# Optimization experiments

Hardware: AMD Instinct MI355X
Metric: run time of the kernel (lower is better)

Reference implementation:

```python
import jax, jax.numpy as jnp
import numpy as np

B, J, O = 32, 20, 20
D, H, F, L = 256, 8, 1024, 6
S = J * O
DH = D // H
NL = L + 1  # 6 encoder blocks + final block stacked together


def setup_inputs() -> dict:
    ks = jax.random.split(jax.random.key(0), 16)
    s = 0.02
    am = jax.random.randint(ks[4], (B, J), 0, 2) == 1
    am = am.at[:, 0].set(False)  # at least one unmasked job per row (avoid all -inf softmax)
    return {
        "operations": jax.random.normal(ks[0], (B, J, O, 2), jnp.float32),
        "job_ops_mask": jax.random.normal(ks[1], (B, J, O, O), jnp.float32),
        "ops_machines_mask": jax.random.normal(ks[2], (B, S, S), jnp.float32),
        "jobs_next_op_idx": jax.random.randint(ks[3], (B, J, 1), 0, O),
        "action_mask": am,
        "qkv_w": jax.random.normal(ks[5], (NL, 3 * D, D), jnp.float32) * s,
        "qkv_b": jnp.zeros((NL, 3 * D), jnp.float32),
        "out_w": jax.random.normal(ks[6], (NL, D, D), jnp.float32) * s,
        "out_b": jnp.zeros((NL, D), jnp.float32),
        "ln1_g": jnp.ones((NL, D), jnp.float32),
        "ln1_b": jnp.zeros((NL, D), jnp.float32),
        "ln2_g": jnp.ones((NL, D), jnp.float32),
        "ln2_b": jnp.zeros((NL, D), jnp.float32),
        "ff1_w": jax.random.normal(ks[7], (NL, F, D), jnp.float32) * s,
        "ff1_b": jnp.zeros((NL, F), jnp.float32),
        "ff2_w": jax.random.normal(ks[8], (NL, D, F), jnp.float32) * s,
        "ff2_b": jnp.zeros((NL, D), jnp.float32),
        "op_emb_w": jax.random.normal(ks[9], (D, 2), jnp.float32) * s,
        "op_emb_b": jnp.zeros((D,), jnp.float32),
        "pol_w": jax.random.normal(ks[10], (1, D), jnp.float32) * s,
        "pol_b": jnp.zeros((1,), jnp.float32),
    }


def _ln(x, g, b):
    m = x.mean(-1, keepdims=True)
    v = ((x - m) ** 2).mean(-1, keepdims=True)
    return (x - m) * jax.lax.rsqrt(v + 1e-5) * g + b


def _mha(x, mask, qw, qb, ow, ob):
    N, Sq, _ = x.shape
    qkv = x @ qw.T + qb
    q, k, v = jnp.split(qkv, 3, axis=-1)
    q = q.reshape(N, Sq, H, DH).transpose(0, 2, 1, 3)
    k = k.reshape(N, Sq, H, DH).transpose(0, 2, 1, 3)
    v = v.reshape(N, Sq, H, DH).transpose(0, 2, 1, 3)
    sc = jnp.einsum("nhqd,nhkd->nhqk", q, k) / jnp.sqrt(jnp.float32(DH))
    sc = sc + mask  # additive float attn mask, broadcast over heads where needed
    a = jax.nn.softmax(sc, axis=-1)
    o = jnp.einsum("nhqk,nhkd->nhqd", a, v).transpose(0, 2, 1, 3).reshape(N, Sq, D)
    return o @ ow.T + ob


def _forward(operations, job_ops_mask, ops_machines_mask, jobs_next_op_idx, action_mask,
             qkv_w, qkv_b, out_w, out_b, ln1_g, ln1_b, ln2_g, ln2_b,
             ff1_w, ff1_b, ff2_w, ff2_b, op_emb_w, op_emb_b, pol_w, pol_b):
    def block(x, mask, i):  # pre-norm TransformerEncoderLayer, gelu, dropout=0
        h = _ln(x, ln1_g[i], ln1_b[i])
        x = x + _mha(h, mask, qkv_w[i], qkv_b[i], out_w[i], out_b[i])
        h = _ln(x, ln2_g[i], ln2_b[i])
        ff = jax.nn.gelu(h @ ff1_w[i].T + ff1_b[i], approximate=False) @ ff2_w[i].T + ff2_b[i]
        return x + ff

    # sinusoidal positional encoding over the operation index
    pos = jnp.arange(O, dtype=jnp.float32)[:, None]
    div = jnp.exp(jnp.arange(0, D, 2, dtype=jnp.float32) * (-np.log(10000.0) / D))
    pe = jnp.stack([jnp.sin(pos * div), jnp.cos(pos * div)], axis=-1).reshape(O, D)
    x = operations @ op_emb_w.T + op_emb_b + pe[None, None]  # (B,J,O,D)

    # ALiBi slopes: 1/x^(i+1), x = 256^(1/H)
    base = (2.0 ** 8) ** (1.0 / H)
    slope = (1.0 / base ** jnp.arange(1, H + 1, dtype=jnp.float32))[None, :, None, None]
    job_mask = job_ops_mask.reshape(B * J, 1, O, O) * slope  # (B*J, H, O, O)
    mach_mask = ops_machines_mask[:, None, :, :]  # (B, 1, S, S), identical across heads

    for i in range(L):
        if i % 2 == 0:  # per-job attention over operations
            x = block(x.reshape(B * J, O, D), job_mask, i).reshape(B, J, O, D)
        else:  # per-machine attention over all operations
            x = block(x.reshape(B, S, D), mach_mask, i).reshape(B, J, O, D)

    idx = jnp.broadcast_to(jobs_next_op_idx[:, :, :, None], (B, J, 1, D))
    nxt = jnp.take_along_axis(x, idx, axis=2)[:, :, 0, :]  # (B, J, D)
    kp = jnp.where(action_mask, -jnp.inf, 0.0)[:, None, None, :]  # key padding mask
    nxt = block(nxt, kp, L)
    logits = (nxt @ pol_w.T + pol_b)[:, :, 0]
    return jnp.where(action_mask, -jnp.inf, logits)


def reference(operations, job_ops_mask, ops_machines_mask, jobs_next_op_idx, action_mask,
              qkv_w, qkv_b, out_w, out_b, ln1_g, ln1_b, ln2_g, ln2_b,
              ff1_w, ff1_b, ff2_w, ff2_b, op_emb_w, op_emb_b, pol_w, pol_b):
    return _forward(operations, job_ops_mask, ops_machines_mask, jobs_next_op_idx, action_mask,
                    qkv_w, qkv_b, out_w, out_b, ln1_g, ln1_b, ln2_g, ln2_b,
                    ff1_w, ff1_b, ff2_w, ff2_b, op_emb_w, op_emb_b, pol_w, pol_b)
```

## Files before the change

kernel.cpp:

```cpp
#include <hip/hip_runtime.h>
#include <math.h>

#define B_  32
#define J_  20
#define O_  20
#define S_  400
#define D_  256
#define H_  8
#define F_  1024
#define L_  6
#define T_  12800
#define T2_ 640

#define NEG_BIG (-1e30f)

typedef __attribute__((ext_vector_type(8))) short short8;
typedef __attribute__((ext_vector_type(4))) float f32x4;

__device__ __forceinline__ short f2b(float f) {
  union { float f; unsigned u; } c; c.f = f;
  unsigned r = (c.u + 0x7FFFu + ((c.u >> 16) & 1u)) >> 16;
  return (short)r;
}
__device__ __forceinline__ float b2f(short s) {
  union { unsigned u; float f; } c;
  c.u = ((unsigned)(unsigned short)s) << 16;
  return c.f;
}
__device__ __forceinline__ unsigned addpk(unsigned a, unsigned b) {
  union { unsigned u; float f; } x, y;
  x.u = a << 16;        y.u = b << 16;        float lo = x.f + y.f;
  x.u = a & 0xffff0000u; y.u = b & 0xffff0000u; float hi = x.f + y.f;
  return (unsigned)(unsigned short)f2b(lo) | ((unsigned)(unsigned short)f2b(hi) << 16);
}
__device__ __forceinline__ void async_copy16(const short* g, short* l) {
  __builtin_amdgcn_global_load_lds(
      (const __attribute__((address_space(1))) void*)g,
      (__attribute__((address_space(3))) void*)l, 16, 0, 0);
}

__global__ __launch_bounds__(256) void k_f2b4(
    const float* __restrict__ s0, short* __restrict__ d0,
    const float* __restrict__ s1, short* __restrict__ d1,
    const float* __restrict__ s2, short* __restrict__ d2,
    const float* __restrict__ s3, short* __restrict__ d3)
{
  int bid = blockIdx.x;
  const float* src; short* dst; int base;
  if (bid < 672)        { src = s0; dst = d0; base = bid; }
  else if (bid < 896)   { src = s1; dst = d1; base = bid - 672; }
  else if (bid < 1792)  { src = s2; dst = d2; base = bid - 896; }
  else                  { src = s3; dst = d3; base = bid - 1792; }
  int i = (base * 256 + threadIdx.x) * 8;
  float4 a = *(const float4*)(src + i);
  float4 b = *(const float4*)(src + i + 4);
  short8 o;
  o[0] = f2b(a.x); o[1] = f2b(a.y); o[2] = f2b(a.z); o[3] = f2b(a.w);
  o[4] = f2b(b.x); o[5] = f2b(b.y); o[6] = f2b(b.z); o[7] = f2b(b.w);
  *(short8*)(dst + i) = o;
}

__global__ __launch_bounds__(640) void k_maskconv(
    const void* __restrict__ am_raw, int* __restrict__ am_out)
{
  __shared__ int isInt32;
  const int tid = threadIdx.x;
  if (tid == 0) isInt32 = 1;
  __syncthreads();
  if (tid < 160) {
    int v = ((const int*)am_raw)[tid];
    if (v != 0 && v != 1) atomicAnd(&isInt32, 0);
  }
  __syncthreads();
  if (tid < 640) {
    int v;
    if (isInt32) v = ((const int*)am_raw)[tid] != 0;
    else         v = ((const unsigned char*)am_raw)[tid] != 0;
    am_out[tid] = v;
  }
}

__global__ __launch_bounds__(256) void k_embed(
    const float* __restrict__ ops, const float* __restrict__ ew,
    const float* __restrict__ eb, short* __restrict__ x)
{
  int idx = blockIdx.x * 256 + threadIdx.x;
  int d = idx & 255;
  int t = idx >> 8;
  int o = t % O_;
  float a0 = ops[(size_t)t * 2 + 0], a1 = ops[(size_t)t * 2 + 1];
  int k = d >> 1;
  float div = expf((float)(2 * k) * -0.03597789207803197f);
  float ang = (float)o * div;
  float pe = (d & 1) ? cosf(ang) : sinf(ang);
  x[idx] = f2b(a0 * ew[d * 2 + 0] + a1 * ew[d * 2 + 1] + eb[d] + pe);
}

__global__ __launch_bounds__(256) void k_ln(
    const short* __restrict__ x, const float* __restrict__ g, const float* __restrict__ b,
    short* __restrict__ out, int nTok)
{
  int gid = blockIdx.x * 256 + threadIdx.x;
  int tok = gid >> 6, lane = threadIdx.x & 63;
  if (tok >= nTok) return;
  int2 pk = ((const int2*)(x + (size_t)tok * 256))[lane];
  union { unsigned u; float f; } c;
  float vx, vy, vz, vw;
  c.u = (unsigned)pk.x << 16;        vx = c.f;
  c.u = (unsigned)pk.x & 0xffff0000u; vy = c.f;
  c.u = (unsigned)pk.y << 16;        vz = c.f;
  c.u = (unsigned)pk.y & 0xffff0000u; vw = c.f;
  float s = vx + vy + vz + vw;
  #pragma unroll
  for (int off = 32; off > 0; off >>= 1) s += __shfl_down(s, off);
  float mean = __shfl(s, 0) * (1.f / 256.f);
  float dx = vx - mean, dy = vy - mean, dz = vz - mean, dw = vw - mean;
  float q = dx * dx + dy * dy + dz * dz + dw * dw;
  #pragma unroll
  for (int off = 32; off > 0; off >>= 1) q += __shfl_down(q, off);
  float var = __shfl(q, 0) * (1.f / 256.f);
  float inv = 1.f / sqrtf(var + 1e-5f);
  float4 gv = ((const float4*)g)[lane];
  float4 bv = ((const float4*)b)[lane];
  float ox = dx * inv * gv.x + bv.x;
  float oy = dy * inv * gv.y + bv.y;
  float oz = dz * inv * gv.z + bv.z;
  float ow = dw * inv * gv.w + bv.w;
  int2 po;
  po.x = (int)(unsigned short)f2b(ox) | ((int)(unsigned short)f2b(oy) << 16);
  po.y = (int)(unsigned short)f2b(oz) | ((int)(unsigned short)f2b(ow) << 16);
  ((int2*)(out + (size_t)tok * 256))[lane] = po;
}

__global__ __launch_bounds__(256) void k_gemm_bf16(
    const short* __restrict__ A, const short* __restrict__ W,
    const float* __restrict__ bias, const short* __restrict__ R,
    short* __restrict__ C, int M, int N, int K, int act)
{
  __shared__ short LDS_[17408];
  short* Asf = LDS_;
  short* Bsf = LDS_ + 8192;
  short* Csf = LDS_;
  const int tid  = threadIdx.x;
  const int lane = tid & 63;
  const int wv   = tid >> 6;
  const int lm   = lane & 15;
  const int quad = lane >> 4;
  const int wm   = (wv >> 1) * 64;
  const int wn   = (wv & 1) * 64;
  const int n0 = blockIdx.x * 128;
  const int m0 = blockIdx.y * 128;

  f32x4 acc[4][4] = {};

  for (int k0 = 0; k0 < K; k0 += 64) {
    __syncthreads();
    #pragma unroll
    for (int i = 0; i < 4; ++i) {
      const int c    = tid + 256 * i;
      const int row  = c >> 3;
      const int kc8  = ((c & 7) ^ (row & 7)) * 8;
      async_copy16(A + (size_t)(m0 + row) * K + k0 + kc8, &Asf[c * 8]);
      async_copy16(W + (size_t)(n0 + row) * K + k0 + kc8, &Bsf[c * 8]);
    }
    __syncthreads();
    #pragma unroll
    for (int kh = 0; kh < 2; ++kh) {
      short8 af[4], bf[4];
      #pragma unroll
      for (int i = 0; i < 4; ++i) {
        const int row  = wm + i * 16 + lm;
        const int slot = (kh * 4 + quad) ^ (lm & 7);
        af[i] = *(short8*)&Asf[(row * 8 + slot) * 8];
      }
      #pragma unroll
      for (int j = 0; j < 4; ++j) {
        const int row  = wn + j * 16 + lm;
        const int slot = (kh * 4 + quad) ^ (lm & 7);
        bf[j] = *(short8*)&Bsf[(row * 8 + slot) * 8];
      }
      #pragma unroll
      for (int i = 0; i < 4; ++i)
        #pragma unroll
        for (int j = 0; j < 4; ++j)
          acc[i][j] = __builtin_amdgcn_mfma_f32_16x16x32_bf16(af[i], bf[j], acc[i][j], 0, 0, 0);
    }
  }

  __syncthreads();
  #pragma unroll
  for (int j = 0; j < 4; ++j) {
    const int ccol = wn + j * 16 + lm;
    const float bv = bias[n0 + ccol];
    #pragma unroll
    for (int i = 0; i < 4; ++i) {
      #pragma unroll
      for (int r = 0; r < 4; ++r) {
        const int row = wm + i * 16 + quad * 4 + r;
        float vvv = acc[i][j][r] + bv;
        if (act) vvv = vvv / (1.f + __expf(-1.702f * vvv));
        Csf[row * 136 + ccol] = f2b(vvv);
      }
    }
  }
  __syncthreads();
  {
    const int srow = tid >> 1, sh = (tid & 1) * 64;
    const size_t gbase = (size_t)(m0 + srow) * N + n0 + sh;
    const short* ls = &Csf[srow * 136 + sh];
    #pragma unroll
    for (int u = 0; u < 8; ++u) {
      uint4 v = *(const uint4*)(ls + u * 8);
      if (R) {
        uint4 rv = *(const uint4*)(R + gbase + u * 8);
        v.x = addpk(v.x, rv.x); v.y = addpk(v.y, rv.y);
        v.z = addpk(v.z, rv.z); v.w = addpk(v.w, rv.w);
      }
      *(uint4*)(C + gbase + u * 8) = v;
    }
  }
}

__global__ __launch_bounds__(256) void k_gemm_ln(
    const short* __restrict__ A, const short* __restrict__ W,
    const float* __restrict__ bias, const short* __restrict__ R,
    short* __restrict__ X, short* __restrict__ Hout,
    const float* __restrict__ g, const float* __restrict__ bb_,
    int M, int K)
{
  __shared__ short LDS_[4096 + 16896];
  short* Asf = LDS_;
  short* Bsf = LDS_ + 4096;
  short* Csf = LDS_ + 4096;
  const int tid  = threadIdx.x;
  const int lane = tid & 63;
  const int wv   = tid >> 6;
  const int lm   = lane & 15;
  const int quad = lane >> 4;
  const int wn   = wv * 64;
  const int m0   = blockIdx.x * 64;

  f32x4 acc[4][4] = {};

  for (int k0 = 0; k0 < K; k0 += 64) {
    __syncthreads();
    #pragma unroll
    for (int i = 0; i < 2; ++i) {
      const int c   = tid + 256 * i;
      const int row = c >> 3;
      const int kc8 = ((c & 7) ^ (row & 7)) * 8;
      async_copy16(A + (size_t)(m0 + row) * K + k0 + kc8, &Asf[c * 8]);
    }
    #pragma unroll
    for (int i = 0; i < 8; ++i) {
      const int c   = tid + 256 * i;
      const int row = c >> 3;
      const int kc8 = ((c & 7) ^ (row & 7)) * 8;
      async_copy16(W + (size_t)row * K + k0 + kc8, &Bsf[c * 8]);
    }
    __syncthreads();
    #pragma unroll
    for (int kh = 0; kh < 2; ++kh) {
      short8 af[4], bf[4];
      #pragma unroll
      for (int i = 0; i < 4; ++i) {
        const int row  = i * 16 + lm;
        const int slot = (kh * 4 + quad) ^ (lm & 7);
        af[i] = *(short8*)&Asf[(row * 8 + slot) * 8];
      }
      #pragma unroll
      for (int j = 0; j < 4; ++j) {
        const int row  = wn + j * 16 + lm;
        const int slot = (kh * 4 + quad) ^ (lm & 7);
        bf[j] = *(short8*)&Bsf[(row * 8 + slot) * 8];
      }
      #pragma unroll
      for (int i = 0; i < 4; ++i)
        #pragma unroll
        for (int j = 0; j < 4; ++j)
          acc[i][j] = __builtin_amdgcn_mfma_f32_16x16x32_bf16(af[i], bf[j], acc[i][j], 0, 0, 0);
    }
  }

  __syncthreads();
  #pragma unroll
  for (int j = 0; j < 4; ++j) {
    const int ccol = wn + j * 16 + lm;
    const float bv = bias[ccol];
    #pragma unroll
    for (int i = 0; i < 4; ++i) {
      #pragma unroll
      for (int r = 0; r < 4; ++r) {
        const int row = i * 16 + quad * 4 + r;
        Csf[row * 264 + ccol] = f2b(acc[i][j][r] + bv);
      }
    }
  }
  __syncthreads();

  {
    const int row = tid >> 2, cb = (tid & 3) * 64;
    const size_t gbase = (size_t)(m0 + row) * 256 + cb;
    const short* ls = &Csf[row * 264 + cb];
    uint4 xv[8];
    float s1 = 0.f, s2 = 0.f;
    #pragma unroll
    for (int u = 0; u < 8; ++u) {
      uint4 v = *(const uint4*)(ls + u * 8);
      uint4 rv = *(const uint4*)(R + gbase + u * 8);
      v.x = addpk(v.x, rv.x); v.y = addpk(v.y, rv.y);
      v.z = addpk(v.z, rv.z); v.w = addpk(v.w, rv.w);
      xv[u] = v;
      *(uint4*)(X + gbase + u * 8) = v;
      #pragma unroll
      for (int w2 = 0; w2 < 4; ++w2) {
        unsigned pv = (&v.x)[w2];
        union { unsigned u; float f; } c1, c2;
        c1.u = pv << 16; c2.u = pv & 0xffff0000u;
        s1 += c1.f + c2.f;
        s2 += c1.f * c1.f + c2.f * c2.f;
      }
    }
    s1 += __shfl_xor(s1, 1); s2 += __shfl_xor(s2, 1);
    s1 += __shfl_xor(s1, 2); s2 += __shfl_xor(s2, 2);
    const float mean = s1 * (1.f / 256.f);
    const float var  = s2 * (1.f / 256.f) - mean * mean;
    const float inv  = 1.f / sqrtf(var + 1e-5f);
    #pragma unroll
    for (int u = 0; u < 8; ++u) {
      float4 g0 = *(const float4*)(g + cb + u * 8);
      float4 g1 = *(const float4*)(g + cb + u * 8 + 4);
      float4 b0 = *(const float4*)(bb_ + cb + u * 8);
      float4 b1 = *(const float4*)(bb_ + cb + u * 8 + 4);
      auto lnpk = [&](unsigned pv, float ga, float gb2, float ba, float bb2) -> unsigned {
        union { unsigned u; float f; } c1, c2;
        c1.u = pv << 16; c2.u = pv & 0xffff0000u;
        float lo = (c1.f - mean) * inv * ga + ba;
        float hi = (c2.f - mean) * inv * gb2 + bb2;
        return (unsigned)(unsigned short)f2b(lo) | ((unsigned)(unsigned short)f2b(hi) << 16);
      };
      uint4 hv;
      hv.x = lnpk(xv[u].x, g0.x, g0.y, b0.x, b0.y);
      hv.y = lnpk(xv[u].y, g0.z, g0.w, b0.z, b0.w);
      hv.z = lnpk(xv[u].z, g1.x, g1.y, b1.x, b1.y);
      hv.w = lnpk(xv[u].w, g1.z, g1.w, b1.z, b1.w);
      *(uint4*)(Hout + gbase + u * 8) = hv;
    }
  }
}

#define QSTR 776
#define PSTR20 40
__global__ __launch_bounds__(512) void k_attn20_mfma(
    const short* __restrict__ qkv, short* __restrict__ att,
    const float* __restrict__ jmask, const int* __restrict__ amask, int mode)
{
  __shared__ short QK[32 * QSTR];
  __shared__ short Ps[8][32 * PSTR20];
  const int seq  = blockIdx.x;
  const int tid  = threadIdx.x;
  const int wv   = tid >> 6;
  const int lane = tid & 63;
  const int l15  = lane & 15;
  const int quad = lane >> 4;
  const float scale = 0.1767766952966369f;

  for (int e = tid; e < 3072; e += 512) {
    int row = e / 96, c8 = (e % 96) * 8;
    uint4 v = {0u, 0u, 0u, 0u};
    if (row < 20) v = *(const uint4*)(qkv + ((size_t)seq * 20 + row) * 768 + c8);
    *(uint4*)&QK[row * QSTR + c8] = v;
  }
  __syncthreads();

  const short8 aq0 = *(short8*)&QK[(0  + l15) * QSTR + wv * 32 + quad * 8];
  const short8 aq1 = *(short8*)&QK[(16 + l15) * QSTR + wv * 32 + quad * 8];
  const short8 bk0 = *(short8*)&QK[(0  + l15) * QSTR + 256 + wv * 32 + quad * 8];
  const short8 bk1 = *(short8*)&QK[(16 + l15) * QSTR + 256 + wv * 32 + quad * 8];
  f32x4 z4 = {0.f, 0.f, 0.f, 0.f};
  f32x4 s00 = __builtin_amdgcn_mfma_f32_16x16x32_bf16(aq0, bk0, z4, 0, 0, 0);
  f32x4 s01 = __builtin_amdgcn_mfma_f32_16x16x32_bf16(aq0, bk1, z4, 0, 0, 0);
  f32x4 s10 = __builtin_amdgcn_mfma_f32_16x16x32_bf16(aq1, bk0, z4, 0, 0, 0);
  f32x4 s11 = __builtin_amdgcn_mfma_f32_16x16x32_bf16(aq1, bk1, z4, 0, 0, 0);

  const float slope = exp2f(-(float)(wv + 1));
  short* psw = &Ps[wv][0];
  float l0[4] = {0.f, 0.f, 0.f, 0.f};
  float l1[4] = {0.f, 0.f, 0.f, 0.f};

  #pragma unroll
  for (int kt = 0; kt < 2; ++kt) {
    const int k  = kt * 16 + l15;
    const int kc = (k < 20) ? k : 19;
    float madd1 = 0.f;
    if (mode == 1) madd1 = amask[seq * 20 + kc] ? NEG_BIG : 0.f;
    #pragma unroll
    for (int qt = 0; qt < 2; ++qt) {
      f32x4 s = (kt == 0) ? (qt == 0 ? s00 : s10) : (qt == 0 ? s01 : s11);
      #pragma unroll
      for (int r = 0; r < 4; ++r) {
        const int q  = qt * 16 + quad * 4 + r;
        const int qc = (q < 20) ? q : 19;
        float sv = s[r] * scale;
        if (mode == 0) sv += jmask[(size_t)seq * 400 + qc * 20 + kc] * slope;
        else           sv += madd1;
        float p = (k < 20) ? __expf(fminf(sv, 40.f)) : 0.f;
        if (qt == 0) l0[r] += p; else l1[r] += p;
        psw[q * PSTR20 + k] = f2b(p);
      }
    }
  }
  #pragma unroll
  for (int r = 0; r < 4; ++r) {
    float t0 = l0[r];
    t0 += __shfl_xor(t0, 1); t0 += __shfl_xor(t0, 2);
    t0 += __shfl_xor(t0, 4); t0 += __shfl_xor(t0, 8);
    l0[r] = 1.f / t0;
    float t1 = l1[r];
    t1 += __shfl_xor(t1, 1); t1 += __shfl_xor(t1, 2);
    t1 += __shfl_xor(t1, 4); t1 += __shfl_xor(t1, 8);
    l1[r] = 1.f / t1;
  }

  const short8 pf0 = *(short8*)&psw[(0  + l15) * PSTR20 + quad * 8];
  const short8 pf1 = *(short8*)&psw[(16 + l15) * PSTR20 + quad * 8];
  #pragma unroll
  for (int dt = 0; dt < 2; ++dt) {
    const int d = wv * 32 + dt * 16 + l15;
    short8 vf;
    #pragma unroll
    for (int j = 0; j < 8; ++j)
      vf[j] = QK[(quad * 8 + j) * QSTR + 512 + d];
    f32x4 o0 = __builtin_amdgcn_mfma_f32_16x16x32_bf16(pf0, vf, z4, 0, 0, 0);
    f32x4 o1 = __builtin_amdgcn_mfma_f32_16x16x32_bf16(pf1, vf, z4, 0, 0, 0);
    #pragma unroll
    for (int r = 0; r < 4; ++r) {
      const int q = quad * 4 + r;
      att[((size_t)seq * 20 + q) * 256 + d] = f2b(o0[r] * l0[r]);
    }
    if (quad == 0) {
      #pragma unroll
      for (int r = 0; r < 4; ++r) {
        const int q = 16 + r;
        att[((size_t)seq * 20 + q) * 256 + d] = f2b(o1[r] * l1[r]);
      }
    }
  }
}

#define KSTR 264
#define PSTR 40
__global__ __launch_bounds__(512) void k_attn400_mfma(
    const short* __restrict__ qkv, short* __restrict__ att,
    const float* __restrict__ mmask)
{
  __shared__ short Ks[32 * KSTR];
  __shared__ short Vs[32 * KSTR];
  __shared__ short Ps[8][16 * PSTR];

  const int id   = blockIdx.x;
  const int b    = (id >> 3) / 25 * 8 + (id & 7);
  const int qt   = (id >> 3) % 25;
  const int tid  = threadIdx.x;
  const int wv   = tid >> 6;
  const int lane = tid & 63;
  const int l15  = lane & 15;
  const int quad = lane >> 4;
  const int q0   = qt * 16;
  const float scale = 0.1767766952966369f;

  short* Qt = &Ps[0][0];
  {
    int row = tid >> 5, ch = tid & 31;
    uint4 v = *(const uint4*)(qkv + ((size_t)b * 400 + q0 + row) * 768 + ch * 8);
    *(uint4*)&Qt[row * KSTR + (ch ^ (row >> 3)) * 8] = v;
  }
  __syncthreads();
  const short8 af = *(short8*)&Qt[l15 * KSTR + ((wv * 4 + quad) ^ (l15 >> 3)) * 8];

  f32x4 accO[2] = {};
  float lrun[4] = {0.f, 0.f, 0.f, 0.f};

  const float* mrow_base = mmask + ((size_t)b * 400 + q0) * 400;

  const int r0_ = tid >> 5,          ch0 = tid & 31;
  const int r1_ = (tid + 512) >> 5,  ch1 = tid & 31;
  const int dst0 = r0_ * KSTR + (ch0 ^ (r0_ >> 3)) * 8;
  const int dst1 = r1_ * KSTR + (ch1 ^ (r1_ >> 3)) * 8;

  uint4 kp0, kp1, vp0, vp1;
  auto loadKV = [&](int k0) {
    uint4 z = {0u, 0u, 0u, 0u};
    int kr0 = k0 + r0_, kr1 = k0 + r1_;
    if (kr0 < 400) {
      const short* p = qkv + ((size_t)b * 400 + kr0) * 768 + 256 + ch0 * 8;
      kp0 = *(const uint4*)p; vp0 = *(const uint4*)(p + 256);
    } else { kp0 = z; vp0 = z; }
    if (kr1 < 400) {
      const short* p = qkv + ((size_t)b * 400 + kr1) * 768 + 256 + ch1 * 8;
      kp1 = *(const uint4*)p; vp1 = *(const uint4*)(p + 256);
    } else { kp1 = z; vp1 = z; }
  };
  float mA[4], mB[4];
  auto loadMask = [&](int k0, float* a, float* bm) {
    const int kA = k0 + l15, kB = k0 + 16 + l15;
    #pragma unroll
    for (int r = 0; r < 4; ++r) {
      const int qrow = quad * 4 + r;
      a[r]  = (kA < 400) ? mrow_base[(size_t)qrow * 400 + kA] : 0.f;
      bm[r] = (kB < 400) ? mrow_base[(size_t)qrow * 400 + kB] : 0.f;
    }
  };

  loadKV(0);
  loadMask(0, mA, mB);
  for (int k0 = 0; k0 < 416; k0 += 32) {
    __syncthreads();
    *(uint4*)&Ks[dst0] = kp0; *(uint4*)&Ks[dst1] = kp1;
    *(uint4*)&Vs[dst0] = vp0; *(uint4*)&Vs[dst1] = vp1;
    float nA[4], nB[4];
    if (k0 + 32 < 416) { loadKV(k0 + 32); loadMask(k0 + 32, nA, nB); }
    __syncthreads();

    const short8 kf0 = *(short8*)&Ks[(0  + l15) * KSTR + (((wv * 4 + quad) ^ (l15 >> 3)) * 8)];
    const short8 kf1 = *(short8*)&Ks[(16 + l15) * KSTR + (((wv * 4 + quad) ^ (2 + (l15 >> 3))) * 8)];
    f32x4 z4 = {0.f, 0.f, 0.f, 0.f};
    f32x4 s0 = __builtin_amdgcn_mfma_f32_16x16x32_bf16(af, kf0, z4, 0, 0, 0);
    f32x4 s1 = __builtin_amdgcn_mfma_f32_16x16x32_bf16(af, kf1, z4, 0, 0, 0);

    const int kA = k0 + l15, kB = k0 + 16 + l15;
    float p0[4], p1[4];
    #pragma unroll
    for (int r = 0; r < 4; ++r) {
      float svA = (kA < 400) ? (s0[r] * scale + mA[r]) : NEG_BIG;
      float svB = (kB < 400) ? (s1[r] * scale + mB[r]) : NEG_BIG;
      p0[r] = __expf(fminf(svA, 40.f));
      p1[r] = __expf(fminf(svB, 40.f));
      float rs = p0[r] + p1[r];
      rs += __shfl_xor(rs, 1);
      rs += __shfl_xor(rs, 2);
      rs += __shfl_xor(rs, 4);
      rs += __shfl_xor(rs, 8);
      lrun[r] += rs;
    }
    #pragma unroll
    for (int r = 0; r < 4; ++r) { mA[r] = nA[r]; mB[r] = nB[r]; }

    short* psw = &Ps[wv][0];
    #pragma unroll
    for (int r = 0; r < 4; ++r) {
      const int qrow = quad * 4 + r;
      psw[qrow * PSTR + l15]      = f2b(p0[r]);
      psw[qrow * PSTR + 16 + l15] = f2b(p1[r]);
    }
    const short8 pf = *(short8*)&psw[l15 * PSTR + quad * 8];

    #pragma unroll
    for (int c = 0; c < 2; ++c) {
      const int dcol = wv * 32 + c * 16 + l15;
      const int base = ((dcol >> 3) ^ quad) * 8 + (dcol & 7);
      short8 vf;
      #pragma unroll
      for (int j = 0; j < 8; ++j)
        vf[j] = Vs[(quad * 8 + j) * KSTR + base];
      accO[c] = __builtin_amdgcn_mfma_f32_16x16x32_bf16(pf, vf, accO[c], 0, 0, 0);
    }
  }

  #pragma unroll
  for (int c = 0; c < 2; ++c) {
    const int dcol = wv * 32 + c * 16 + l15;
    #pragma unroll
    for (int r = 0; r < 4; ++r) {
      float o = accO[c][r] / lrun[r];
      att[((size_t)b * 400 + q0 + quad * 4 + r) * 256 + dcol] = f2b(o);
    }
  }
}

__global__ __launch_bounds__(256) void k_gather2(
    const short* __restrict__ x, const short* __restrict__ h,
    const int* __restrict__ idx, short* __restrict__ x2, short* __restrict__ h2)
{
  int t = blockIdx.x * 256 + threadIdx.x;
  if (t >= 640 * 16) return;
  int bj = t >> 4, c = t & 15;
  int o = idx[bj];
  size_t src = ((size_t)bj * 20 + o) * 256;
  ((uint4*)(x2 + (size_t)bj * 256))[c] = ((const uint4*)(x + src))[c];
  ((uint4*)(h2 + (size_t)bj * 256))[c] = ((const uint4*)(h + src))[c];
}

__global__ __launch_bounds__(256) void k_logits(
    const short* __restrict__ x2, const float* __restrict__ pw, const float* __restrict__ pb,
    const int* __restrict__ am, float* __restrict__ out)
{
  int gid = blockIdx.x * 256 + threadIdx.x;
  int row = gid >> 6, lane = threadIdx.x & 63;
  int2 pk = ((const int2*)(x2 + (size_t)row * 256))[lane];
  union { unsigned u; float f; } c;
  float vx, vy, vz, vw;
  c.u = (unsigned)pk.x << 16;         vx = c.f;
  c.u = (unsigned)pk.x & 0xffff0000u; vy = c.f;
  c.u = (unsigned)pk.y << 16;         vz = c.f;
  c.u = (unsigned)pk.y & 0xffff0000u; vw = c.f;
  float4 w = ((const float4*)pw)[lane];
  float s = vx * w.x + vy * w.y + vz * w.z + vw * w.w;
  #pragma unroll
  for (int off = 32; off > 0; off >>= 1) s += __shfl_down(s, off);
  if (lane == 0) out[row] = am[row] ? NEG_BIG : (s + pb[0]);
}

extern "C" void kernel_launch(void* const* d_in, const int* in_sizes, int n_in,
                              void* d_out, int out_size, void* d_ws, size_t ws_size,
                              hipStream_t stream)
{
  (void)in_sizes; (void)n_in; (void)out_size; (void)ws_size;
  const float* operations        = (const float*)d_in[0];
  const float* job_ops_mask      = (const float*)d_in[1];
  const float* ops_machines_mask = (const float*)d_in[2];
  const int*   jobs_next_op_idx  = (const int*)d_in[3];
  const void*  action_mask_raw   = (const void*)d_in[4];
  const float* qkv_w = (const float*)d_in[5];
  const float* qkv_b = (const float*)d_in[6];
  const float* out_w = (const float*)d_in[7];
  const float* out_b = (const float*)d_in[8];
  const float* ln1_g = (const float*)d_in[9];
  const float* ln1_b = (const float*)d_in[10];
  const float* ln2_g = (const float*)d_in[11];
  const float* ln2_b = (const float*)d_in[12];
  const float* ff1_w = (const float*)d_in[13];
  const float* ff1_b = (const float*)d_in[14];
  const float* ff2_w = (const float*)d_in[15];
  const float* ff2_b = (const float*)d_in[16];
  const float* op_emb_w = (const float*)d_in[17];
  const float* op_emb_b = (const float*)d_in[18];
  const float* pol_w = (const float*)d_in[19];
  const float* pol_b = (const float*)d_in[20];
  float* out = (float*)d_out;

  short* x    = (short*)d_ws;
  short* x2   = x + (size_t)T_ * D_;
  short* h    = x2 + (size_t)T2_ * D_;
  short* big  = h + (size_t)T_ * D_;
  short* h2   = big + (size_t)T_ * F_;
  short* big2 = h2 + (size_t)T2_ * D_;
  int*   amc  = (int*)(big2 + (size_t)T2_ * F_);
  short* bwq  = (short*)(amc + 640);
  short* bwo  = bwq + (size_t)7 * 768 * 256;
  short* bwf1 = bwo + (size_t)7 * 256 * 256;
  short* bwf2 = bwf1 + (size_t)7 * 1024 * 256;

  auto gemm = [&](const short* A, const short* Wb, const float* bias, const short* R,
                  short* C, int M, int N, int K, int act) {
    k_gemm_bf16<<<dim3(N / 128, M / 128), dim3(256), 0, stream>>>(
        A, Wb, bias, R, C, M, N, K, act);
  };
  auto gemm_ln = [&](const short* A, const short* Wb, const float* bias, const short* R,
                     short* X, short* Hout, const float* g, const float* b, int M, int K) {
    k_gemm_ln<<<dim3(M / 64), dim3(256), 0, stream>>>(
        A, Wb, bias, R, X, Hout, g, b, M, K);
  };

  k_f2b4<<<dim3(2688), 256, 0, stream>>>(qkv_w, bwq, out_w, bwo, ff1_w, bwf1, ff2_w, bwf2);
  k_maskconv<<<dim3(1), dim3(640), 0, stream>>>(action_mask_raw, amc);
  k_embed<<<dim3(T_ * D_ / 256), dim3(256), 0, stream>>>(operations, op_emb_w, op_emb_b, x);
  k_ln<<<dim3(T_ / 4), 256, 0, stream>>>(x, ln1_g, ln1_b, h, T_);

  for (int i = 0; i < L_; ++i) {
    const short* qw  = bwq  + (size_t)i * 768 * 256;
    const float* qb  = qkv_b + (size_t)i * 768;
    const short* ow  = bwo  + (size_t)i * 256 * 256;
    const float* ob  = out_b + (size_t)i * 256;
    const short* f1w = bwf1 + (size_t)i * 1024 * 256;
    const float* f1b = ff1_b + (size_t)i * 1024;
    const short* f2w = bwf2 + (size_t)i * 256 * 1024;
    const float* f2b_ = ff2_b + (size_t)i * 256;
    gemm(h, qw, qb, nullptr, big, T_, 768, 256, 0);
    if ((i & 1) == 0)
      k_attn20_mfma<<<dim3(640), 512, 0, stream>>>(big, h, job_ops_mask, nullptr, 0);
    else
      k_attn400_mfma<<<dim3(800), 512, 0, stream>>>(big, h, ops_machines_mask);
    gemm_ln(h, ow, ob, x, x, h, ln2_g + i * D_, ln2_b + i * D_, T_, 256);
    gemm(h, f1w, f1b, nullptr, big, T_, 1024, 256, 1);
    gemm_ln(big, f2w, f2b_, x, x, h, ln1_g + (i + 1) * D_, ln1_b + (i + 1) * D_, T_, 1024);
  }

  k_gather2<<<dim3(40), 256, 0, stream>>>(x, h, jobs_next_op_idx, x2, h2);

  {
    int i = L_;
    const short* qw  = bwq  + (size_t)i * 768 * 256;
    const float* qb  = qkv_b + (size_t)i * 768;
    const short* ow  = bwo  + (size_t)i * 256 * 256;
    const float* ob  = out_b + (size_t)i * 256;
    const short* f1w = bwf1 + (size_t)i * 1024 * 256;
    const float* f1b = ff1_b + (size_t)i * 1024;
    const short* f2w = bwf2 + (size_t)i * 256 * 1024;
    const float* f2b_ = ff2_b + (size_t)i * 256;
    gemm(h2, qw, qb, nullptr, big2, T2_, 768, 256, 0);
    k_attn20_mfma<<<dim3(32), 512, 0, stream>>>(big2, h2, nullptr, amc, 1);
    gemm_ln(h2, ow, ob, x2, x2, h2, ln2_g + i * D_, ln2_b + i * D_, T2_, 256);
    gemm(h2, f1w, f1b, nullptr, big2, T2_, 1024, 256, 1);
    gemm(big2, f2w, f2b_, x2, x2, T2_, 256, 1024, 0);
  }

  k_logits<<<dim3(160), 256, 0, stream>>>(x2, pol_w, pol_b, amc, out);
}
```

Before: 1.016 ms.

## Fuse FFN up-projection, activation, down-projection and LayerNorm into one kernel

Replaces the two FFN GEMM launches with one kernel. Each 32-row tile keeps its hidden activations in LDS in 256-column chunks and feeds them straight into the second GEMM, then applies bias, residual add and the next LayerNorm. This removes the global-memory round trip of the 12800x1024 hidden tensor and one launch per layer. In exchange, the small M tile reads every weight once per block, and with only 400 blocks of 256 threads occupancy is low and the barrier-heavy pipeline may limit MFMA throughput.

```diff
diff --git a/kernel.cpp b/kernel.cpp
--- a/kernel.cpp
+++ b/kernel.cpp
@@ -345,6 +345,183 @@
       hv.z = lnpk(xv[u].z, g1.x, g1.y, b1.x, b1.y);
       hv.w = lnpk(xv[u].w, g1.z, g1.w, b1.z, b1.w);
       *(uint4*)(Hout + gbase + u * 8) = hv;
+    }
+  }
+}
+
+__global__ __launch_bounds__(256) void k_ffn(
+    const short* __restrict__ A, const short* __restrict__ W1, const float* __restrict__ b1,
+    const short* __restrict__ W2, const float* __restrict__ b2, const short* __restrict__ R,
+    short* __restrict__ X, short* __restrict__ Hout,
+    const float* __restrict__ g, const float* __restrict__ bb_)
+{
+  __shared__ short LDS_[32768];
+  short* Ah  = LDS_;
+  short* Bsf = LDS_ + 8192;
+  short* Hs  = LDS_ + 24576;
+  const int tid  = threadIdx.x;
+  const int lane = tid & 63;
+  const int wv   = tid >> 6;
+  const int lm   = lane & 15;
+  const int quad = lane >> 4;
+  const int wn   = wv * 64;
+  const int m0   = blockIdx.x * 32;
+
+  #pragma unroll
+  for (int i = 0; i < 4; ++i) {
+    int c = tid + 256 * i;
+    int row = c >> 5, gch = c & 31;
+    uint4 v = *(const uint4*)(A + (size_t)(m0 + row) * 256 + gch * 8);
+    *(uint4*)&Ah[row * 256 + ((gch ^ (row & 7)) * 8)] = v;
+  }
+
+  uint4 wreg[8];
+  auto prefetch = [&](int p) {
+    const int c = p >> 3, sub = (p >> 2) & 1, k0 = (p & 3) * 64;
+    #pragma unroll
+    for (int i = 0; i < 8; ++i) {
+      const int cc = tid + 256 * i;
+      const int row = cc >> 3;
+      const int xc = ((cc & 7) ^ (row & 7)) * 8;
+      const short* src = (sub == 0)
+        ? W1 + ((size_t)(c * 256 + row)) * 256 + k0 + xc
+        : W2 + (size_t)row * 1024 + c * 256 + k0 + xc;
+      wreg[i] = *(const uint4*)src;
+    }
+  };
+
+  prefetch(0);
+  f32x4 oacc[2][4] = {};
+  f32x4 hacc[2][4];
+  const f32x4 z4 = {0.f, 0.f, 0.f, 0.f};
+
+  for (int p = 0; p < 32; ++p) {
+    const int c = p >> 3, sub = (p >> 2) & 1, k0 = (p & 3) * 64;
+    __syncthreads();
+    #pragma unroll
+    for (int i = 0; i < 8; ++i) *(uint4*)&Bsf[(tid + 256 * i) * 8] = wreg[i];
+    if (p + 1 < 32) prefetch(p + 1);
+    __syncthreads();
+    if (sub == 0 && (p & 3) == 0) {
+      #pragma unroll
+      for (int i = 0; i < 2; ++i)
+        #pragma unroll
+        for (int j = 0; j < 4; ++j) hacc[i][j] = z4;
+    }
+    const short* Asrc = (sub == 0) ? Ah : Hs;
+    #pragma unroll
+    for (int kh = 0; kh < 2; ++kh) {
+      short8 af[2], bf[4];
+      #pragma unroll
+      for (int i = 0; i < 2; ++i) {
+        const int row = i * 16 + lm;
+        const int slot = ((k0 >> 3) + kh * 4 + quad) ^ (row & 7);
+        af[i] = *(short8*)&Asrc[row * 256 + slot * 8];
+      }
+      #pragma unroll
+      for (int j = 0; j < 4; ++j) {
+        const int row = wn + j * 16 + lm;
+        const int slot = (kh * 4 + quad) ^ (lm & 7);
+        bf[j] = *(short8*)&Bsf[(row * 8 + slot) * 8];
+      }
+      if (sub == 0) {
+        #pragma unroll
+        for (int i = 0; i < 2; ++i)
+          #pragma unroll
+          for (int j = 0; j < 4; ++j)
+            hacc[i][j] = __builtin_amdgcn_mfma_f32_16x16x32_bf16(af[i], bf[j], hacc[i][j], 0, 0, 0);
+      } else {
+        #pragma unroll
+        for (int i = 0; i < 2; ++i)
+          #pragma unroll
+          for (int j = 0; j < 4; ++j)
+            oacc[i][j] = __builtin_amdgcn_mfma_f32_16x16x32_bf16(af[i], bf[j], oacc[i][j], 0, 0, 0);
+      }
+    }
+    if (sub == 0 && (p & 3) == 3) {
+      #pragma unroll
+      for (int j = 0; j < 4; ++j) {
+        const int col = wn + j * 16 + lm;
+        const float bv = b1[c * 256 + col];
+        #pragma unroll
+        for (int i = 0; i < 2; ++i)
+          #pragma unroll
+          for (int rr = 0; rr < 4; ++rr) {
+            const int row = i * 16 + quad * 4 + rr;
+            float v = hacc[i][j][rr] + bv;
+            v = v / (1.f + __expf(-1.702f * v));
+            const int slot = (col >> 3) ^ (row & 7);
+            Hs[row * 256 + slot * 8 + (col & 7)] = f2b(v);
+          }
+      }
+    }
+  }
+
+  __syncthreads();
+  #pragma unroll
+  for (int j = 0; j < 4; ++j) {
+    const int col = wn + j * 16 + lm;
+    const float bv = b2[col];
+    #pragma unroll
+    for (int i = 0; i < 2; ++i)
+      #pragma unroll
+      for (int rr = 0; rr < 4; ++rr) {
+        const int row = i * 16 + quad * 4 + rr;
+        const int slot = (col >> 3) ^ (row & 7);
+        Hs[row * 256 + slot * 8 + (col & 7)] = f2b(oacc[i][j][rr] + bv);
+      }
+  }
+  __syncthreads();
+  {
+    const int row = tid >> 3, cb = (tid & 7) * 32;
+    const size_t gbase = (size_t)(m0 + row) * 256 + cb;
+    uint4 xv[4];
+    float s1 = 0.f, s2 = 0.f;
+    #pragma unroll
+    for (int u = 0; u < 4; ++u) {
+      const int slot = ((cb >> 3) + u) ^ (row & 7);
+      uint4 v = *(const uint4*)&Hs[row * 256 + slot * 8];
+      uint4 rv = *(const uint4*)(R + gbase + u * 8);
+      v.x = addpk(v.x, rv.x); v.y = addpk(v.y, rv.y);
+      v.z = addpk(v.z, rv.z); v.w = addpk(v.w, rv.w);
+      xv[u] = v;
+      *(uint4*)(X + gbase + u * 8) = v;
+      #pragma unroll
+      for (int w2 = 0; w2 < 4; ++w2) {
+        unsigned pv = (&v.x)[w2];
+        union { unsigned u; float f; } c1, c2;
+        c1.u = pv << 16; c2.u = pv & 0xffff0000u;
+        s1 += c1.f + c2.f;
+        s2 += c1.f * c1.f + c2.f * c2.f;
+      }
+    }
+    s1 += __shfl_xor(s1, 1); s2 += __shfl_xor(s2, 1);
+    s1 += __shfl_xor(s1, 2); s2 += __shfl_xor(s2, 2);
+    s1 += __shfl_xor(s1, 4); s2 += __shfl_xor(s2, 4);
+    if (g) {
+      const float mean = s1 * (1.f / 256.f);
+      const float var  = s2 * (1.f / 256.f) - mean * mean;
+      const float inv  = 1.f / sqrtf(var + 1e-5f);
+      #pragma unroll
+      for (int u = 0; u < 4; ++u) {
+        float4 g0 = *(const float4*)(g + cb + u * 8);
+        float4 g1 = *(const float4*)(g + cb + u * 8 + 4);
+        float4 b0 = *(const float4*)(bb_ + cb + u * 8);
+        float4 b1v = *(const float4*)(bb_ + cb + u * 8 + 4);
+        auto lnpk = [&](unsigned pv, float ga, float gb2, float ba, float bb2) -> unsigned {
+          union { unsigned u; float f; } c1, c2;
+          c1.u = pv << 16; c2.u = pv & 0xffff0000u;
+          float lo = (c1.f - mean) * inv * ga + ba;
+          float hi = (c2.f - mean) * inv * gb2 + bb2;
+          return (unsigned)(unsigned short)f2b(lo) | ((unsigned)(unsigned short)f2b(hi) << 16);
+        };
+        uint4 hv;
+        hv.x = lnpk(xv[u].x, g0.x, g0.y, b0.x, b0.y);
+        hv.y = lnpk(xv[u].y, g0.z, g0.w, b0.z, b0.w);
+        hv.z = lnpk(xv[u].z, g1.x, g1.y, b1v.x, b1v.y);
+        hv.w = lnpk(xv[u].w, g1.z, g1.w, b1v.z, b1v.w);
+        *(uint4*)(Hout + gbase + u * 8) = hv;
+      }
     }
   }
 }
@@ -682,8 +859,9 @@
     else
       k_attn400_mfma<<<dim3(800), 512, 0, stream>>>(big, h, ops_machines_mask);
     gemm_ln(h, ow, ob, x, x, h, ln2_g + i * D_, ln2_b + i * D_, T_, 256);
-    gemm(h, f1w, f1b, nullptr, big, T_, 1024, 256, 1);
-    gemm_ln(big, f2w, f2b_, x, x, h, ln1_g + (i + 1) * D_, ln1_b + (i + 1) * D_, T_, 1024);
+    k_ffn<<<dim3(T_ / 32), dim3(256), 0, stream>>>(
+        h, f1w, f1b, f2w, f2b_, x, x, h,
+        ln1_g + (i + 1) * D_, ln1_b + (i + 1) * D_);
   }
 
   k_gather2<<<dim3(40), 256, 0, stream>>>(x, h, jobs_next_op_idx, x2, h2);
@@ -701,8 +879,8 @@
     gemm(h2, qw, qb, nullptr, big2, T2_, 768, 256, 0);
     k_attn20_mfma<<<dim3(32), 512, 0, stream>>>(big2, h2, nullptr, amc, 1);
     gemm_ln(h2, ow, ob, x2, x2, h2, ln2_g + i * D_, ln2_b + i * D_, T2_, 256);
-    gemm(h2, f1w, f1b, nullptr, big2, T2_, 1024, 256, 1);
-    gemm(big2, f2w, f2b_, x2, x2, T2_, 256, 1024, 0);
+    k_ffn<<<dim3(T2_ / 32), dim3(256), 0, stream>>>(
+        h2, f1w, f1b, f2w, f2b_, x2, x2, nullptr, nullptr, nullptr);
   }
 
   k_logits<<<dim3(160), 256, 0, stream>>>(x2, pol_w, pol_b, amc, out);
```

After: 1.588 ms. 1.56x slower.

## Load K per-wave into registers and stage V per-wave to drop block barriers

Applied to the files above, without the earlier changes.

Each wave now reads its own head's Q and K fragments directly from global memory, prefetching the next tile's K and mask into registers. Only that wave's V slice is staged, in a private LDS region. This removes the block-wide shared K/V tiles and both __syncthreads per key tile, so waves proceed independently. The cost is more direct global loads with less coalescing, and reads past row 400 on the last tile that depend on masking for correctness.

```diff
diff --git a/kernel.cpp b/kernel.cpp
--- a/kernel.cpp
+++ b/kernel.cpp
@@ -448,15 +448,13 @@
   }
 }
 
-#define KSTR 264
-#define PSTR 40
+#define VSTR 36
+#define PSTRW 40
 __global__ __launch_bounds__(512) void k_attn400_mfma(
     const short* __restrict__ qkv, short* __restrict__ att,
     const float* __restrict__ mmask)
 {
-  __shared__ short Ks[32 * KSTR];
-  __shared__ short Vs[32 * KSTR];
-  __shared__ short Ps[8][16 * PSTR];
+  __shared__ short Wl[8 * 1792];
 
   const int id   = blockIdx.x;
   const int b    = (id >> 3) / 25 * 8 + (id & 7);
@@ -469,71 +467,57 @@
   const int q0   = qt * 16;
   const float scale = 0.1767766952966369f;
 
-  short* Qt = &Ps[0][0];
-  {
-    int row = tid >> 5, ch = tid & 31;
-    uint4 v = *(const uint4*)(qkv + ((size_t)b * 400 + q0 + row) * 768 + ch * 8);
-    *(uint4*)&Qt[row * KSTR + (ch ^ (row >> 3)) * 8] = v;
-  }
-  __syncthreads();
-  const short8 af = *(short8*)&Qt[l15 * KSTR + ((wv * 4 + quad) ^ (l15 >> 3)) * 8];
+  short* Vw = &Wl[wv * 1792];
+  short* Pw = &Wl[wv * 1792 + 1152];
+  const short* qbase = qkv + (size_t)b * 400 * 768;
+
+  const short8 af = *(const short8*)(qbase + (size_t)(q0 + l15) * 768 + wv * 32 + quad * 8);
 
   f32x4 accO[2] = {};
   float lrun[4] = {0.f, 0.f, 0.f, 0.f};
-
   const float* mrow_base = mmask + ((size_t)b * 400 + q0) * 400;
 
-  const int r0_ = tid >> 5,          ch0 = tid & 31;
-  const int r1_ = (tid + 512) >> 5,  ch1 = tid & 31;
-  const int dst0 = r0_ * KSTR + (ch0 ^ (r0_ >> 3)) * 8;
-  const int dst1 = r1_ * KSTR + (ch1 ^ (r1_ >> 3)) * 8;
-
-  uint4 kp0, kp1, vp0, vp1;
-  auto loadKV = [&](int k0) {
-    uint4 z = {0u, 0u, 0u, 0u};
-    int kr0 = k0 + r0_, kr1 = k0 + r1_;
-    if (kr0 < 400) {
-      const short* p = qkv + ((size_t)b * 400 + kr0) * 768 + 256 + ch0 * 8;
-      kp0 = *(const uint4*)p; vp0 = *(const uint4*)(p + 256);
-    } else { kp0 = z; vp0 = z; }
-    if (kr1 < 400) {
-      const short* p = qkv + ((size_t)b * 400 + kr1) * 768 + 256 + ch1 * 8;
-      kp1 = *(const uint4*)p; vp1 = *(const uint4*)(p + 256);
-    } else { kp1 = z; vp1 = z; }
-  };
+  const int vrow = lane >> 1;
+  const int vch  = (lane & 1) * 2;
+  const int vdst = vrow * VSTR + vch * 8;
+
+  short8 kf0, kf1;
   float mA[4], mB[4];
-  auto loadMask = [&](int k0, float* a, float* bm) {
+  auto prefKM = [&](int k0) {
+    kf0 = *(const short8*)(qbase + (size_t)(k0 + l15) * 768 + 256 + wv * 32 + quad * 8);
+    kf1 = *(const short8*)(qbase + (size_t)(k0 + 16 + l15) * 768 + 256 + wv * 32 + quad * 8);
     const int kA = k0 + l15, kB = k0 + 16 + l15;
     #pragma unroll
     for (int r = 0; r < 4; ++r) {
       const int qrow = quad * 4 + r;
-      a[r]  = (kA < 400) ? mrow_base[(size_t)qrow * 400 + kA] : 0.f;
-      bm[r] = (kB < 400) ? mrow_base[(size_t)qrow * 400 + kB] : 0.f;
+      mA[r] = mrow_base[(size_t)qrow * 400 + kA];
+      mB[r] = (kB < 400) ? mrow_base[(size_t)qrow * 400 + kB] : 0.f;
     }
   };
-
-  loadKV(0);
-  loadMask(0, mA, mB);
+  prefKM(0);
+
   for (int k0 = 0; k0 < 416; k0 += 32) {
-    __syncthreads();
-    *(uint4*)&Ks[dst0] = kp0; *(uint4*)&Ks[dst1] = kp1;
-    *(uint4*)&Vs[dst0] = vp0; *(uint4*)&Vs[dst1] = vp1;
-    float nA[4], nB[4];
-    if (k0 + 32 < 416) { loadKV(k0 + 32); loadMask(k0 + 32, nA, nB); }
-    __syncthreads();
-
-    const short8 kf0 = *(short8*)&Ks[(0  + l15) * KSTR + (((wv * 4 + quad) ^ (l15 >> 3)) * 8)];
-    const short8 kf1 = *(short8*)&Ks[(16 + l15) * KSTR + (((wv * 4 + quad) ^ (2 + (l15 >> 3))) * 8)];
+    const short* vp = qbase + (size_t)(k0 + vrow) * 768 + 512 + wv * 32 + vch * 8;
+    const uint4 v0 = *(const uint4*)vp;
+    const uint4 v1 = *(const uint4*)(vp + 8);
+
+    const short8 ck0 = kf0, ck1 = kf1;
+    float cA[4], cB[4];
+    #pragma unroll
+    for (int r = 0; r < 4; ++r) { cA[r] = mA[r]; cB[r] = mB[r]; }
+
     f32x4 z4 = {0.f, 0.f, 0.f, 0.f};
-    f32x4 s0 = __builtin_amdgcn_mfma_f32_16x16x32_bf16(af, kf0, z4, 0, 0, 0);
-    f32x4 s1 = __builtin_amdgcn_mfma_f32_16x16x32_bf16(af, kf1, z4, 0, 0, 0);
-
-    const int kA = k0 + l15, kB = k0 + 16 + l15;
+    f32x4 s0 = __builtin_amdgcn_mfma_f32_16x16x32_bf16(af, ck0, z4, 0, 0, 0);
+    f32x4 s1 = __builtin_amdgcn_mfma_f32_16x16x32_bf16(af, ck1, z4, 0, 0, 0);
+
+    if (k0 + 32 < 416) prefKM(k0 + 32);
+
+    const int kB = k0 + 16 + l15;
     float p0[4], p1[4];
     #pragma unroll
     for (int r = 0; r < 4; ++r) {
-      float svA = (kA < 400) ? (s0[r] * scale + mA[r]) : NEG_BIG;
-      float svB = (kB < 400) ? (s1[r] * scale + mB[r]) : NEG_BIG;
+      float svA = s0[r] * scale + cA[r];
+      float svB = (kB < 400) ? (s1[r] * scale + cB[r]) : NEG_BIG;
       p0[r] = __expf(fminf(svA, 40.f));
       p1[r] = __expf(fminf(svB, 40.f));
       float rs = p0[r] + p1[r];
@@ -543,26 +527,23 @@
       rs += __shfl_xor(rs, 8);
       lrun[r] += rs;
     }
-    #pragma unroll
-    for (int r = 0; r < 4; ++r) { mA[r] = nA[r]; mB[r] = nB[r]; }
-
-    short* psw = &Ps[wv][0];
+
     #pragma unroll
     for (int r = 0; r < 4; ++r) {
       const int qrow = quad * 4 + r;
-      psw[qrow * PSTR + l15]      = f2b(p0[r]);
-      psw[qrow * PSTR + 16 + l15] = f2b(p1[r]);
-    }
-    const short8 pf = *(short8*)&psw[l15 * PSTR + quad * 8];
-
+      Pw[qrow * PSTRW + l15]      = f2b(p0[r]);
+      Pw[qrow * PSTRW + 16 + l15] = f2b(p1[r]);
+    }
+    const short8 pf = *(short8*)&Pw[l15 * PSTRW + quad * 8];
+
+    *(uint4*)&Vw[vdst]     = v0;
+    *(uint4*)&Vw[vdst + 8] = v1;
     #pragma unroll
     for (int c = 0; c < 2; ++c) {
-      const int dcol = wv * 32 + c * 16 + l15;
-      const int base = ((dcol >> 3) ^ quad) * 8 + (dcol & 7);
       short8 vf;
       #pragma unroll
       for (int j = 0; j < 8; ++j)
-        vf[j] = Vs[(quad * 8 + j) * KSTR + base];
+        vf[j] = Vw[(quad * 8 + j) * VSTR + c * 16 + l15];
       accO[c] = __builtin_amdgcn_mfma_f32_16x16x32_bf16(pf, vf, accO[c], 0, 0, 0);
     }
   }
```

After: 1.023 ms. Within noise of the previous version (+0.8%).
